# Kernel tuning notes

Measured on AMD Instinct MI355X. Metric: run time of the kernel, lower is better.

Reference implementation:

```python
import jax, jax.numpy as jnp
import numpy as np

B, S, H, NH, I = 8, 1024, 1024, 16, 4096
HD = H // NH
EPS = 1e-6
NEG = -1e9


def _glorot(key, shape):
    lim = np.sqrt(6.0 / (shape[0] + shape[1]))
    return jax.random.uniform(key, shape, jnp.float32, -lim, lim)


def setup_inputs() -> dict:
    key = jax.random.key(0)
    ks = jax.random.split(key, 8)
    return {
        "inputs": jax.random.normal(ks[0], (B, S, H), jnp.float32),
        "inputs_mask": jnp.zeros((B, S), jnp.float32),  # 1.0 marks padding
        "attn_qkvw": _glorot(ks[1], (H, 3 * H)),
        "attn_qkvb": jnp.zeros((3 * H,), jnp.float32),
        "attn_ow": _glorot(ks[2], (H, H)),
        "attn_ob": jnp.zeros((H,), jnp.float32),
        "attn_nw": jnp.ones((H,), jnp.float32),
        "attn_nb": jnp.zeros((H,), jnp.float32),
        "inter_w": _glorot(ks[3], (H, I)),
        "inter_b": jnp.zeros((I,), jnp.float32),
        "output_w": _glorot(ks[4], (I, H)),
        "output_b": jnp.zeros((H,), jnp.float32),
        "ffn_nw": jnp.ones((H,), jnp.float32),
        "ffn_nb": jnp.zeros((H,), jnp.float32),
    }


def _layer_norm(x, g, b):
    m = jnp.mean(x, axis=-1, keepdims=True)
    v = jnp.mean(jnp.square(x - m), axis=-1, keepdims=True)
    return (x - m) * jax.lax.rsqrt(v + EPS) * g + b


def reference(inputs, inputs_mask, attn_qkvw, attn_qkvb, attn_ow, attn_ob,
              attn_nw, attn_nb, inter_w, inter_b, output_w, output_b,
              ffn_nw, ffn_nb):
    # ---- self-attention block (pre-LN) ----
    res = inputs
    x = _layer_norm(inputs, attn_nw, attn_nb)
    qkv = x @ attn_qkvw + attn_qkvb                      # [B,S,3H]
    q, k, v = jnp.split(qkv, 3, axis=-1)
    q = q.reshape(B, S, NH, HD)
    k = k.reshape(B, S, NH, HD)
    v = v.reshape(B, S, NH, HD)
    scale = 1.0 / np.sqrt(HD)
    scores = jnp.einsum("bqhd,bkhd->bhqk", q, k) * scale
    scores = scores + inputs_mask[:, None, None, :] * NEG
    probs = jax.nn.softmax(scores, axis=-1)
    ctx = jnp.einsum("bhqk,bkhd->bqhd", probs, v).reshape(B, S, H)
    attn_out = ctx @ attn_ow + attn_ob
    x = res + attn_out
    # ---- FFN block (pre-LN, ReLU) ----
    res2 = x
    y = _layer_norm(x, ffn_nw, ffn_nb)
    h = jax.nn.relu(y @ inter_w + inter_b)
    return res2 + h @ output_w + output_b
```

## Files before the change

### kernel.cpp

```cpp
#include <hip/hip_runtime.h>
#include <cstdint>
#include <cstddef>

typedef _Float16 f16;
typedef _Float16 half8 __attribute__((ext_vector_type(8)));
typedef _Float16 half4v __attribute__((ext_vector_type(4)));
typedef float floatx4 __attribute__((ext_vector_type(4)));
typedef float floatx16 __attribute__((ext_vector_type(16)));

__device__ __forceinline__ floatx4 mfma16(half8 a, half8 b, floatx4 c) {
    return __builtin_amdgcn_mfma_f32_16x16x32_f16(a, b, c, 0, 0, 0);
}
__device__ __forceinline__ floatx16 mfma32(half8 a, half8 b, floatx16 c) {
    return __builtin_amdgcn_mfma_f32_32x32x16_f16(a, b, c, 0, 0, 0);
}

__device__ __forceinline__ void async16(const f16* g, f16* l) {
    __builtin_amdgcn_global_load_lds(
        (const __attribute__((address_space(1))) unsigned int*)(uintptr_t)g,
        (__attribute__((address_space(3))) unsigned int*)(uintptr_t)l,
        16, 0, 0);
}

__global__ __launch_bounds__(256)
void ln_f16_kernel(const float* __restrict__ x, const float* __restrict__ g,
                   const float* __restrict__ be, f16* __restrict__ y)
{
    int row = blockIdx.x, t = threadIdx.x;
    const float* xr = x + (size_t)row * 1024;
    float4 v = *(const float4*)(xr + t * 4);
    float s1 = v.x + v.y + v.z + v.w;
    float s2 = v.x * v.x + v.y * v.y + v.z * v.z + v.w * v.w;
    #pragma unroll
    for (int off = 32; off >= 1; off >>= 1) {
        s1 += __shfl_xor(s1, off);
        s2 += __shfl_xor(s2, off);
    }
    __shared__ float r1[4], r2[4];
    if ((t & 63) == 0) { r1[t >> 6] = s1; r2[t >> 6] = s2; }
    __syncthreads();
    s1 = r1[0] + r1[1] + r1[2] + r1[3];
    s2 = r2[0] + r2[1] + r2[2] + r2[3];
    float mean = s1 * 0.0009765625f;
    float var  = s2 * 0.0009765625f - mean * mean;
    float rs = rsqrtf(var + 1e-6f);
    float4 gv = *(const float4*)(g + t * 4);
    float4 bv = *(const float4*)(be + t * 4);
    half4v o;
    o[0] = (f16)((v.x - mean) * rs * gv.x + bv.x);
    o[1] = (f16)((v.y - mean) * rs * gv.y + bv.y);
    o[2] = (f16)((v.z - mean) * rs * gv.z + bv.z);
    o[3] = (f16)((v.w - mean) * rs * gv.w + bv.w);
    *(half4v*)(y + (size_t)row * 1024 + t * 4) = o;
}

__global__ __launch_bounds__(256)
void transpose_f16_kernel(const float* __restrict__ W, f16* __restrict__ WT,
                          int R, int C)
{
    __shared__ float tile[32][33];
    int tx = threadIdx.x & 31, ty0 = threadIdx.x >> 5;
    int r0 = blockIdx.y * 32, c0 = blockIdx.x * 32;
    #pragma unroll
    for (int i = 0; i < 4; ++i)
        tile[ty0 + i * 8][tx] = W[(size_t)(r0 + ty0 + i * 8) * C + c0 + tx];
    __syncthreads();
    #pragma unroll
    for (int i = 0; i < 4; ++i)
        WT[(size_t)(c0 + ty0 + i * 8) * R + r0 + tx] = (f16)tile[tx][ty0 + i * 8];
}

__global__ __launch_bounds__(256, 2)
void gemm_kernel(const f16* __restrict__ A, const f16* __restrict__ BT,
                 const float* __restrict__ bias, const float* __restrict__ res,
                 float* __restrict__ Cf32, int M, int N, int K)
{
    __shared__ __align__(16) f16 As[128 * 64];
    __shared__ __align__(16) f16 Bs[128 * 64];
    int m0 = blockIdx.x * 128, n0 = blockIdx.y * 128;
    int t = threadIdx.x, lane = t & 63, wave = t >> 6;
    int quad = lane >> 4, l16 = lane & 15;
    int wm = (wave & 1) * 64, wn = (wave >> 1) * 64;
    int sw = l16 & 7;
    floatx4 acc[4][4] = {};

    for (int k0 = 0; k0 < K; k0 += 64) {
        __syncthreads();
        #pragma unroll
        for (int c = 0; c < 4; ++c) {
            int s = c * 256 + t;
            int row = s >> 3, phys = s & 7;
            int lg = phys ^ (row & 7);
            async16(A  + (size_t)(m0 + row) * K + k0 + lg * 8,
                    As + (size_t)(c * 256 + (t & ~63)) * 8);
            async16(BT + (size_t)(n0 + row) * K + k0 + lg * 8,
                    Bs + (size_t)(c * 256 + (t & ~63)) * 8);
        }
        __syncthreads();
        #pragma unroll
        for (int ks = 0; ks < 2; ++ks) {
            int ca = (ks * 4 + quad) ^ sw;
            half8 a[4], b[4];
            #pragma unroll
            for (int i = 0; i < 4; ++i) {
                a[i] = *(const half8*)(As + (wm + i * 16 + l16) * 64 + ca * 8);
                b[i] = *(const half8*)(Bs + (wn + i * 16 + l16) * 64 + ca * 8);
            }
            #pragma unroll
            for (int i = 0; i < 4; ++i)
                #pragma unroll
                for (int j = 0; j < 4; ++j)
                    acc[i][j] = mfma16(a[i], b[j], acc[i][j]);
        }
    }

    #pragma unroll
    for (int j = 0; j < 4; ++j) {
        int col = n0 + wn + j * 16 + l16;
        float bv = bias[col];
        #pragma unroll
        for (int i = 0; i < 4; ++i) {
            int rowb = m0 + wm + i * 16 + quad * 4;
            #pragma unroll
            for (int r = 0; r < 4; ++r) {
                float v = acc[i][j][r] + bv;
                size_t idx = (size_t)(rowb + r) * N + col;
                Cf32[idx] = v + res[idx];
            }
        }
    }
}

template<int MODE>
__global__ __launch_bounds__(256, 2)
void gemm_big_kernel(const f16* __restrict__ A, const f16* __restrict__ BT,
                     const float* __restrict__ bias, f16* __restrict__ Cf16,
                     f16* __restrict__ qb, f16* __restrict__ kb, f16* __restrict__ vb,
                     int M, int N, int K)
{
    __shared__ __align__(16) f16 As[256 * 64];
    __shared__ __align__(16) f16 Bs[128 * 64];
    int m0 = blockIdx.x * 256, n0 = blockIdx.y * 128;
    int t = threadIdx.x, lane = t & 63, wave = t >> 6;
    int l32 = lane & 31, kg = lane >> 5;
    int swz = l32 & 7;
    floatx16 acc[2][4];
    #pragma unroll
    for (int mi = 0; mi < 2; ++mi)
        #pragma unroll
        for (int jn = 0; jn < 4; ++jn)
            #pragma unroll
            for (int r = 0; r < 16; ++r) acc[mi][jn][r] = 0.f;

    for (int k0 = 0; k0 < K; k0 += 64) {
        __syncthreads();
        #pragma unroll
        for (int c = 0; c < 8; ++c) {
            int s = c * 256 + t;
            int row = s >> 3, phys = s & 7;
            int lg = phys ^ (row & 7);
            async16(A + (size_t)(m0 + row) * K + k0 + lg * 8,
                    As + (size_t)(c * 256 + (t & ~63)) * 8);
        }
        #pragma unroll
        for (int c = 0; c < 4; ++c) {
            int s = c * 256 + t;
            int row = s >> 3, phys = s & 7;
            int lg = phys ^ (row & 7);
            async16(BT + (size_t)(n0 + row) * K + k0 + lg * 8,
                    Bs + (size_t)(c * 256 + (t & ~63)) * 8);
        }
        __syncthreads();
        #pragma unroll
        for (int ss = 0; ss < 4; ++ss) {
            int ca = (ss * 2 + kg) ^ swz;
            half8 a[2], b[4];
            #pragma unroll
            for (int mi = 0; mi < 2; ++mi)
                a[mi] = *(const half8*)(As + (wave * 64 + mi * 32 + l32) * 64 + ca * 8);
            #pragma unroll
            for (int jn = 0; jn < 4; ++jn)
                b[jn] = *(const half8*)(Bs + (jn * 32 + l32) * 64 + ca * 8);
            #pragma unroll
            for (int mi = 0; mi < 2; ++mi)
                #pragma unroll
                for (int jn = 0; jn < 4; ++jn)
                    acc[mi][jn] = mfma32(a[mi], b[jn], acc[mi][jn]);
        }
    }

    #pragma unroll
    for (int mi = 0; mi < 2; ++mi) {
        int mbase = m0 + wave * 64 + mi * 32 + 4 * kg;
        #pragma unroll
        for (int jn = 0; jn < 4; ++jn) {
            int col = n0 + jn * 32 + l32;
            float bv = bias[col];
            if (MODE == 1) {
                #pragma unroll
                for (int reg = 0; reg < 16; ++reg) {
                    int row = mbase + (reg & 3) + 8 * (reg >> 2);
                    Cf16[(size_t)row * N + col] = (f16)fmaxf(acc[mi][jn][reg] + bv, 0.f);
                }
            } else {
                int part = col >> 10;
                int h = (col >> 6) & 15;
                int d = col & 63;
                if (part == 2) {
                    #pragma unroll
                    for (int rb = 0; rb < 4; ++rb) {
                        int m = mbase + 8 * rb;
                        int bb = m >> 10, s = m & 1023;
                        size_t bh = (size_t)bb * 16 + h;
                        half4v pv;
                        #pragma unroll
                        for (int r = 0; r < 4; ++r) pv[r] = (f16)(acc[mi][jn][rb * 4 + r] + bv);
                        *(half4v*)(vb + (bh * 64 + d) * 1024 + s) = pv;
                    }
                } else {
                    f16* dst0 = part == 0 ? qb : kb;
                    #pragma unroll
                    for (int reg = 0; reg < 16; ++reg) {
                        int m = mbase + (reg & 3) + 8 * (reg >> 2);
                        int bb = m >> 10, s = m & 1023;
                        size_t bh = (size_t)bb * 16 + h;
                        dst0[(bh * 1024 + s) * 64 + d] = (f16)(acc[mi][jn][reg] + bv);
                    }
                }
            }
        }
    }
}

__global__ __launch_bounds__(256)
void attn_kernel(const f16* __restrict__ qb, const f16* __restrict__ kb,
                 const f16* __restrict__ vb, const float* __restrict__ mask,
                 f16* __restrict__ ctx)
{
    const int S = 1024;
    int qt = blockIdx.x, h = blockIdx.y, b = blockIdx.z;
    size_t bh = (size_t)b * 16 + h;
    int t = threadIdx.x, lane = t & 63, wv = t >> 6;
    int quad = lane >> 4, l16 = lane & 15;
    int sw = l16 & 7;

    __shared__ __align__(16) f16 Ks[64 * 64];
    __shared__ __align__(16) f16 Vs[64 * 64];
    __shared__ __align__(16) f16 Ps[4][16 * 40];

    int q0 = qt * 64 + wv * 16;
    const f16* qrow = qb + (bh * 1024 + q0 + l16) * 64;
    half8 aq0 = *(const half8*)(qrow + quad * 8);
    half8 aq1 = *(const half8*)(qrow + 32 + quad * 8);

    floatx4 o[4] = {};
    float lsum[4] = {0.f, 0.f, 0.f, 0.f};
    const float scale = 0.125f;
    const float* mrow = mask + b * S;

    for (int kc = 0; kc < S; kc += 64) {
        __syncthreads();
        #pragma unroll
        for (int c = 0; c < 2; ++c) {
            int s = c * 256 + t;
            int row = s >> 3, phys = s & 7;
            int lg = phys ^ (row & 7);
            f16* lk = Ks + (size_t)(c * 256 + (t & ~63)) * 8;
            f16* lv = Vs + (size_t)(c * 256 + (t & ~63)) * 8;
            async16(kb + (bh * 1024 + kc + row) * 64 + lg * 8, lk);
            async16(vb + (bh * 64 + row) * 1024 + kc + lg * 8, lv);
        }
        __syncthreads();

        floatx4 sf[4];
        #pragma unroll
        for (int cg = 0; cg < 4; ++cg) {
            const f16* kr = Ks + (cg * 16 + l16) * 64;
            int c0 = quad ^ sw;
            half8 b0 = *(const half8*)(kr + c0 * 8);
            half8 b1 = *(const half8*)(kr + (c0 ^ 4) * 8);
            floatx4 z = {};
            sf[cg] = mfma16(aq1, b1, mfma16(aq0, b0, z));
        }
        #pragma unroll
        for (int cg = 0; cg < 4; ++cg) {
            float mk = mrow[kc + cg * 16 + l16] * (-1e9f);
            #pragma unroll
            for (int r = 0; r < 4; ++r) {
                float e = __expf(sf[cg][r] * scale + mk);
                lsum[r] += e;
                Ps[wv][(quad * 4 + r) * 40 + cg * 16 + l16] = (f16)e;
            }
        }
        half8 ap0 = *(const half8*)(Ps[wv] + l16 * 40 + quad * 8);
        half8 ap1 = *(const half8*)(Ps[wv] + l16 * 40 + 32 + quad * 8);
        #pragma unroll
        for (int td = 0; td < 4; ++td) {
            const f16* vr = Vs + (td * 16 + l16) * 64;
            int c0 = quad ^ sw;
            half8 bv0 = *(const half8*)(vr + c0 * 8);
            half8 bv1 = *(const half8*)(vr + (c0 ^ 4) * 8);
            o[td] = mfma16(ap0, bv0, o[td]);
            o[td] = mfma16(ap1, bv1, o[td]);
        }
    }

    #pragma unroll
    for (int r = 0; r < 4; ++r) {
        float s = lsum[r];
        s += __shfl_xor(s, 1); s += __shfl_xor(s, 2);
        s += __shfl_xor(s, 4); s += __shfl_xor(s, 8);
        lsum[r] = 1.f / s;
    }
    #pragma unroll
    for (int td = 0; td < 4; ++td)
        #pragma unroll
        for (int r = 0; r < 4; ++r)
            ctx[((size_t)b * 1024 + q0 + quad * 4 + r) * 1024 + h * 64 + td * 16 + l16]
                = (f16)(o[td][r] * lsum[r]);
}

extern "C" void kernel_launch(void* const* d_in, const int* in_sizes, int n_in,
                              void* d_out, int out_size, void* d_ws, size_t ws_size,
                              hipStream_t stream)
{
    const float* inputs = (const float*)d_in[0];
    const float* mask   = (const float*)d_in[1];
    const float* qkvw   = (const float*)d_in[2];
    const float* qkvb   = (const float*)d_in[3];
    const float* ow     = (const float*)d_in[4];
    const float* ob     = (const float*)d_in[5];
    const float* anw    = (const float*)d_in[6];
    const float* anb    = (const float*)d_in[7];
    const float* iw     = (const float*)d_in[8];
    const float* ib     = (const float*)d_in[9];
    const float* outw   = (const float*)d_in[10];
    const float* outb   = (const float*)d_in[11];
    const float* fnw    = (const float*)d_in[12];
    const float* fnb    = (const float*)d_in[13];
    float* out = (float*)d_out;

    const int M = 8192;
    uint8_t* ws = (uint8_t*)d_ws;
    f16* wT_qkv = (f16*)(ws + 0);
    f16* wT_o   = (f16*)(ws + 6291456);
    f16* wT_i   = (f16*)(ws + 8388608);
    f16* wT_out = (f16*)(ws + 16777216);
    f16* xln    = (f16*)(ws + 25165824);
    float* x1   = (float*)(ws + 41943040);
    f16* qbuf   = (f16*)(ws + 75497472);
    f16* kbuf   = (f16*)(ws + 92274688);
    f16* vbuf   = (f16*)(ws + 109051904);
    f16* ctx    = (f16*)(ws + 125829120);
    f16* hbuf   = (f16*)(ws + 75497472);

    transpose_f16_kernel<<<dim3(96, 32),  256, 0, stream>>>(qkvw, wT_qkv, 1024, 3072);
    transpose_f16_kernel<<<dim3(32, 32),  256, 0, stream>>>(ow,   wT_o,   1024, 1024);
    transpose_f16_kernel<<<dim3(128, 32), 256, 0, stream>>>(iw,   wT_i,   1024, 4096);
    transpose_f16_kernel<<<dim3(32, 128), 256, 0, stream>>>(outw, wT_out, 4096, 1024);

    ln_f16_kernel<<<8192, 256, 0, stream>>>(inputs, anw, anb, xln);

    gemm_big_kernel<2><<<dim3(32, 24), 256, 0, stream>>>(xln, wT_qkv, qkvb,
        nullptr, qbuf, kbuf, vbuf, M, 3072, 1024);

    attn_kernel<<<dim3(16, 16, 8), 256, 0, stream>>>(qbuf, kbuf, vbuf, mask, ctx);

    gemm_kernel<<<dim3(64, 8), 256, 0, stream>>>(ctx, wT_o, ob, inputs,
        x1, M, 1024, 1024);

    ln_f16_kernel<<<8192, 256, 0, stream>>>(x1, fnw, fnb, xln);

    gemm_big_kernel<1><<<dim3(32, 32), 256, 0, stream>>>(xln, wT_i, ib,
        hbuf, nullptr, nullptr, nullptr, M, 4096, 1024);

    gemm_kernel<<<dim3(64, 8), 256, 0, stream>>>(hbuf, wT_out, outb, x1,
        out, M, 1024, 4096);
}
```

Before: 482.3 us.

## Replace GEMMs with triple-buffered 512-thread pipelined MFMA kernel

Replaces both GEMM kernels with one templated kernel that uses 8 waves, a 256x128 tile and a three-stage LDS ring. Async global-to-LDS loads for tile k+2 are interleaved with the MFMA phases of tile k, using explicit barriers, setprio and waitcnt. The aim is to hide global load latency that the old load-sync-compute loop exposed, and to unify the epilogues. In exchange it uses more LDS per block (144KB with three stages), which may limit occupancy, and the hand-placed barriers and waitcnts add synchronisation risk. The output-projection GEMMs now launch fewer, larger blocks (256), which may underfill the CUs.

```diff
diff --git a/kernel.cpp b/kernel.cpp
--- a/kernel.cpp
+++ b/kernel.cpp
@@ -70,160 +70,144 @@
         WT[(size_t)(c0 + ty0 + i * 8) * R + r0 + tx] = (f16)tile[tx][ty0 + i * 8];
 }
 
-__global__ __launch_bounds__(256, 2)
-void gemm_kernel(const f16* __restrict__ A, const f16* __restrict__ BT,
-                 const float* __restrict__ bias, const float* __restrict__ res,
-                 float* __restrict__ Cf32, int M, int N, int K)
-{
-    __shared__ __align__(16) f16 As[128 * 64];
-    __shared__ __align__(16) f16 Bs[128 * 64];
-    int m0 = blockIdx.x * 128, n0 = blockIdx.y * 128;
-    int t = threadIdx.x, lane = t & 63, wave = t >> 6;
-    int quad = lane >> 4, l16 = lane & 15;
-    int wm = (wave & 1) * 64, wn = (wave >> 1) * 64;
-    int sw = l16 & 7;
-    floatx4 acc[4][4] = {};
-
-    for (int k0 = 0; k0 < K; k0 += 64) {
-        __syncthreads();
-        #pragma unroll
-        for (int c = 0; c < 4; ++c) {
-            int s = c * 256 + t;
-            int row = s >> 3, phys = s & 7;
-            int lg = phys ^ (row & 7);
-            async16(A  + (size_t)(m0 + row) * K + k0 + lg * 8,
-                    As + (size_t)(c * 256 + (t & ~63)) * 8);
-            async16(BT + (size_t)(n0 + row) * K + k0 + lg * 8,
-                    Bs + (size_t)(c * 256 + (t & ~63)) * 8);
-        }
-        __syncthreads();
-        #pragma unroll
-        for (int ks = 0; ks < 2; ++ks) {
-            int ca = (ks * 4 + quad) ^ sw;
-            half8 a[4], b[4];
+#define GPHASE(aoff, boff, ss, ...) do {                                        \
+    const int ci_ = ((ss) * 2 + kg) ^ swz;                                      \
+    half8 fa0 = *(const half8*)(AS + (aoff) + (wm +      l32) * 64 + ci_ * 8);  \
+    half8 fa1 = *(const half8*)(AS + (aoff) + (wm + 32 + l32) * 64 + ci_ * 8);  \
+    half8 fb0 = *(const half8*)(BS + (boff) + (wn +      l32) * 64 + ci_ * 8);  \
+    half8 fb1 = *(const half8*)(BS + (boff) + (wn + 32 + l32) * 64 + ci_ * 8);  \
+    __VA_ARGS__                                                                 \
+    __builtin_amdgcn_s_barrier();                                               \
+    asm volatile("s_waitcnt lgkmcnt(0)" ::: "memory");                          \
+    __builtin_amdgcn_sched_barrier(0);                                          \
+    __builtin_amdgcn_s_setprio(1);                                              \
+    acc[0][0] = mfma32(fa0, fb0, acc[0][0]);                                    \
+    acc[0][1] = mfma32(fa0, fb1, acc[0][1]);                                    \
+    acc[1][0] = mfma32(fa1, fb0, acc[1][0]);                                    \
+    acc[1][1] = mfma32(fa1, fb1, acc[1][1]);                                    \
+    __builtin_amdgcn_s_setprio(0);                                              \
+    __builtin_amdgcn_s_barrier();                                               \
+} while (0)
+
+template<int MODE>
+__global__ __launch_bounds__(512, 2)
+void gemm_pipe_kernel(const f16* __restrict__ A, const f16* __restrict__ BT,
+                      const float* __restrict__ bias, const float* __restrict__ res,
+                      float* __restrict__ Cf32, f16* __restrict__ Cf16,
+                      f16* __restrict__ qb, f16* __restrict__ kb, f16* __restrict__ vb,
+                      int M, int N, int K)
+{
+    __shared__ __align__(16) f16 AS[3 * 256 * 64];
+    __shared__ __align__(16) f16 BS[3 * 128 * 64];
+    const int m0 = blockIdx.x * 256, n0 = blockIdx.y * 128;
+    const int t = threadIdx.x, lane = t & 63, wave = t >> 6;
+    const int l32 = lane & 31, kg = lane >> 5, swz = l32 & 7;
+    const int wm = (wave >> 1) * 64, wn = (wave & 1) * 64;
+
+    floatx16 acc[2][2];
+    #pragma unroll
+    for (int i = 0; i < 2; ++i)
+        #pragma unroll
+        for (int j = 0; j < 2; ++j)
             #pragma unroll
-            for (int i = 0; i < 4; ++i) {
-                a[i] = *(const half8*)(As + (wm + i * 16 + l16) * 64 + ca * 8);
-                b[i] = *(const half8*)(Bs + (wn + i * 16 + l16) * 64 + ca * 8);
-            }
-            #pragma unroll
-            for (int i = 0; i < 4; ++i)
-                #pragma unroll
-                for (int j = 0; j < 4; ++j)
-                    acc[i][j] = mfma16(a[i], b[j], acc[i][j]);
-        }
-    }
-
-    #pragma unroll
-    for (int j = 0; j < 4; ++j) {
-        int col = n0 + wn + j * 16 + l16;
-        float bv = bias[col];
-        #pragma unroll
-        for (int i = 0; i < 4; ++i) {
-            int rowb = m0 + wm + i * 16 + quad * 4;
-            #pragma unroll
-            for (int r = 0; r < 4; ++r) {
-                float v = acc[i][j][r] + bv;
-                size_t idx = (size_t)(rowb + r) * N + col;
-                Cf32[idx] = v + res[idx];
-            }
-        }
-    }
-}
-
-template<int MODE>
-__global__ __launch_bounds__(256, 2)
-void gemm_big_kernel(const f16* __restrict__ A, const f16* __restrict__ BT,
-                     const float* __restrict__ bias, f16* __restrict__ Cf16,
-                     f16* __restrict__ qb, f16* __restrict__ kb, f16* __restrict__ vb,
-                     int M, int N, int K)
-{
-    __shared__ __align__(16) f16 As[256 * 64];
-    __shared__ __align__(16) f16 Bs[128 * 64];
-    int m0 = blockIdx.x * 256, n0 = blockIdx.y * 128;
-    int t = threadIdx.x, lane = t & 63, wave = t >> 6;
-    int l32 = lane & 31, kg = lane >> 5;
-    int swz = l32 & 7;
-    floatx16 acc[2][4];
-    #pragma unroll
-    for (int mi = 0; mi < 2; ++mi)
-        #pragma unroll
-        for (int jn = 0; jn < 4; ++jn)
-            #pragma unroll
-            for (int r = 0; r < 16; ++r) acc[mi][jn][r] = 0.f;
-
-    for (int k0 = 0; k0 < K; k0 += 64) {
-        __syncthreads();
-        #pragma unroll
-        for (int c = 0; c < 8; ++c) {
-            int s = c * 256 + t;
-            int row = s >> 3, phys = s & 7;
-            int lg = phys ^ (row & 7);
-            async16(A + (size_t)(m0 + row) * K + k0 + lg * 8,
-                    As + (size_t)(c * 256 + (t & ~63)) * 8);
-        }
-        #pragma unroll
-        for (int c = 0; c < 4; ++c) {
-            int s = c * 256 + t;
-            int row = s >> 3, phys = s & 7;
-            int lg = phys ^ (row & 7);
-            async16(BT + (size_t)(n0 + row) * K + k0 + lg * 8,
-                    Bs + (size_t)(c * 256 + (t & ~63)) * 8);
-        }
-        __syncthreads();
-        #pragma unroll
-        for (int ss = 0; ss < 4; ++ss) {
-            int ca = (ss * 2 + kg) ^ swz;
-            half8 a[2], b[4];
-            #pragma unroll
-            for (int mi = 0; mi < 2; ++mi)
-                a[mi] = *(const half8*)(As + (wave * 64 + mi * 32 + l32) * 64 + ca * 8);
-            #pragma unroll
-            for (int jn = 0; jn < 4; ++jn)
-                b[jn] = *(const half8*)(Bs + (jn * 32 + l32) * 64 + ca * 8);
-            #pragma unroll
-            for (int mi = 0; mi < 2; ++mi)
-                #pragma unroll
-                for (int jn = 0; jn < 4; ++jn)
-                    acc[mi][jn] = mfma32(a[mi], b[jn], acc[mi][jn]);
-        }
-    }
+            for (int r = 0; r < 16; ++r) acc[i][j][r] = 0.f;
+
+    const f16* gA[4]; int oA[4];
+    #pragma unroll
+    for (int c = 0; c < 4; ++c) {
+        int s = c * 512 + t, row = s >> 3, lg = (s & 7) ^ (row & 7);
+        gA[c] = A + (size_t)(m0 + row) * K + lg * 8;
+        oA[c] = (c * 512 + (t & ~63)) * 8;
+    }
+    const f16* gB[2]; int oB[2];
+    #pragma unroll
+    for (int c = 0; c < 2; ++c) {
+        int s = c * 512 + t, row = s >> 3, lg = (s & 7) ^ (row & 7);
+        gB[c] = BT + (size_t)(n0 + row) * K + lg * 8;
+        oB[c] = (c * 512 + (t & ~63)) * 8;
+    }
+
+    int ac = 0, an = 16384, as_ = 32768;
+    int bc = 0, bn = 8192,  bs_ = 16384;
+
+    #pragma unroll
+    for (int c = 0; c < 4; ++c) async16(gA[c], AS + ac + oA[c]);
+    #pragma unroll
+    for (int c = 0; c < 2; ++c) async16(gB[c], BS + bc + oB[c]);
+    #pragma unroll
+    for (int c = 0; c < 4; ++c) async16(gA[c] + 64, AS + an + oA[c]);
+    #pragma unroll
+    for (int c = 0; c < 2; ++c) async16(gB[c] + 64, BS + bn + oB[c]);
+    asm volatile("s_waitcnt vmcnt(6)" ::: "memory");
+    __builtin_amdgcn_s_barrier();
+
+    const int NT = K >> 6;
+    #pragma unroll 1
+    for (int it = 0; it < NT - 2; ++it) {
+        const int k2 = (it + 2) << 6;
+        GPHASE(ac, bc, 0, async16(gA[0] + k2, AS + as_ + oA[0]);
+                          async16(gA[1] + k2, AS + as_ + oA[1]); );
+        GPHASE(ac, bc, 1, async16(gA[2] + k2, AS + as_ + oA[2]);
+                          async16(gA[3] + k2, AS + as_ + oA[3]); );
+        GPHASE(ac, bc, 2, async16(gB[0] + k2, BS + bs_ + oB[0]);
+                          async16(gB[1] + k2, BS + bs_ + oB[1]); );
+        GPHASE(ac, bc, 3, );
+        asm volatile("s_waitcnt vmcnt(6)" ::: "memory");
+        __builtin_amdgcn_s_barrier();
+        int tp = ac; ac = an; an = as_; as_ = tp;
+        tp = bc; bc = bn; bn = bs_; bs_ = tp;
+    }
+    GPHASE(ac, bc, 0, ); GPHASE(ac, bc, 1, );
+    GPHASE(ac, bc, 2, ); GPHASE(ac, bc, 3, );
+    asm volatile("s_waitcnt vmcnt(0)" ::: "memory");
+    __builtin_amdgcn_s_barrier();
+    ac = an; bc = bn;
+    GPHASE(ac, bc, 0, ); GPHASE(ac, bc, 1, );
+    GPHASE(ac, bc, 2, ); GPHASE(ac, bc, 3, );
 
     #pragma unroll
     for (int mi = 0; mi < 2; ++mi) {
-        int mbase = m0 + wave * 64 + mi * 32 + 4 * kg;
-        #pragma unroll
-        for (int jn = 0; jn < 4; ++jn) {
-            int col = n0 + jn * 32 + l32;
-            float bv = bias[col];
-            if (MODE == 1) {
+        const int mbase = m0 + wm + mi * 32 + 4 * kg;
+        #pragma unroll
+        for (int jn = 0; jn < 2; ++jn) {
+            const int col = n0 + wn + jn * 32 + l32;
+            const float bv = bias[col];
+            if (MODE == 0) {
                 #pragma unroll
                 for (int reg = 0; reg < 16; ++reg) {
-                    int row = mbase + (reg & 3) + 8 * (reg >> 2);
+                    const int row = mbase + (reg & 3) + 8 * (reg >> 2);
+                    const size_t idx = (size_t)row * N + col;
+                    Cf32[idx] = acc[mi][jn][reg] + bv + res[idx];
+                }
+            } else if (MODE == 1) {
+                #pragma unroll
+                for (int reg = 0; reg < 16; ++reg) {
+                    const int row = mbase + (reg & 3) + 8 * (reg >> 2);
                     Cf16[(size_t)row * N + col] = (f16)fmaxf(acc[mi][jn][reg] + bv, 0.f);
                 }
             } else {
-                int part = col >> 10;
-                int h = (col >> 6) & 15;
-                int d = col & 63;
+                const int part = col >> 10;
+                const int h = (col >> 6) & 15;
+                const int d = col & 63;
                 if (part == 2) {
                     #pragma unroll
                     for (int rb = 0; rb < 4; ++rb) {
-                        int m = mbase + 8 * rb;
-                        int bb = m >> 10, s = m & 1023;
-                        size_t bh = (size_t)bb * 16 + h;
+                        const int m = mbase + 8 * rb;
+                        const int bb = m >> 10, s = m & 1023;
+                        const size_t bh = (size_t)bb * 16 + h;
                         half4v pv;
                         #pragma unroll
-                        for (int r = 0; r < 4; ++r) pv[r] = (f16)(acc[mi][jn][rb * 4 + r] + bv);
+                        for (int r = 0; r < 4; ++r)
+                            pv[r] = (f16)(acc[mi][jn][rb * 4 + r] + bv);
                         *(half4v*)(vb + (bh * 64 + d) * 1024 + s) = pv;
                     }
                 } else {
                     f16* dst0 = part == 0 ? qb : kb;
                     #pragma unroll
                     for (int reg = 0; reg < 16; ++reg) {
-                        int m = mbase + (reg & 3) + 8 * (reg >> 2);
-                        int bb = m >> 10, s = m & 1023;
-                        size_t bh = (size_t)bb * 16 + h;
+                        const int m = mbase + (reg & 3) + 8 * (reg >> 2);
+                        const int bb = m >> 10, s = m & 1023;
+                        const size_t bh = (size_t)bb * 16 + h;
                         dst0[(bh * 1024 + s) * 64 + d] = (f16)(acc[mi][jn][reg] + bv);
                     }
                 }
@@ -361,19 +345,19 @@
 
     ln_f16_kernel<<<8192, 256, 0, stream>>>(inputs, anw, anb, xln);
 
-    gemm_big_kernel<2><<<dim3(32, 24), 256, 0, stream>>>(xln, wT_qkv, qkvb,
-        nullptr, qbuf, kbuf, vbuf, M, 3072, 1024);
+    gemm_pipe_kernel<2><<<dim3(32, 24), 512, 0, stream>>>(xln, wT_qkv, qkvb,
+        nullptr, nullptr, nullptr, qbuf, kbuf, vbuf, M, 3072, 1024);
 
     attn_kernel<<<dim3(16, 16, 8), 256, 0, stream>>>(qbuf, kbuf, vbuf, mask, ctx);
 
-    gemm_kernel<<<dim3(64, 8), 256, 0, stream>>>(ctx, wT_o, ob, inputs,
-        x1, M, 1024, 1024);
+    gemm_pipe_kernel<0><<<dim3(32, 8), 512, 0, stream>>>(ctx, wT_o, ob, inputs,
+        x1, nullptr, nullptr, nullptr, nullptr, M, 1024, 1024);
 
     ln_f16_kernel<<<8192, 256, 0, stream>>>(x1, fnw, fnb, xln);
 
-    gemm_big_kernel<1><<<dim3(32, 32), 256, 0, stream>>>(xln, wT_i, ib,
-        hbuf, nullptr, nullptr, nullptr, M, 4096, 1024);
-
-    gemm_kernel<<<dim3(64, 8), 256, 0, stream>>>(hbuf, wT_out, outb, x1,
-        out, M, 1024, 4096);
-}
+    gemm_pipe_kernel<1><<<dim3(32, 32), 512, 0, stream>>>(xln, wT_i, ib,
+        nullptr, nullptr, hbuf, nullptr, nullptr, nullptr, M, 4096, 1024);
+
+    gemm_pipe_kernel<0><<<dim3(32, 8), 512, 0, stream>>>(hbuf, wT_out, outb, x1,
+        out, nullptr, nullptr, nullptr, nullptr, M, 1024, 4096);
+}
```

New measurement: 489.8 us. Within noise of the previous version (+1.6%).

## Pre-pack B weights into MFMA fragment layout and load them straight into registers

Applied to the files above, without the earlier changes.

Adds a packing kernel that converts the output-projection and FFN-output weights into per-lane MFMA fragment order. A new GEMM kernel then loads B fragments from global memory directly into registers, no longer staging B through LDS. This halves LDS traffic and shared memory per block for those two GEMMs. In exchange, each wave now reads its B fragments from global or L2 memory without reuse across the two M-waves. Those loads are also not overlapped with the LDS staging and could add latency.

```diff
diff --git a/kernel.cpp b/kernel.cpp
--- a/kernel.cpp
+++ b/kernel.cpp
@@ -70,47 +70,82 @@
         WT[(size_t)(c0 + ty0 + i * 8) * R + r0 + tx] = (f16)tile[tx][ty0 + i * 8];
 }
 
+__global__ __launch_bounds__(256)
+void pack_b_kernel(const float* __restrict__ W, f16* __restrict__ Bp, int K, int N)
+{
+    __shared__ float tile[64][65];
+    int n00 = blockIdx.x * 64, k00 = blockIdx.y * 64;
+    int t = threadIdx.x;
+    int tx = t & 63, r0 = t >> 6;
+    #pragma unroll
+    for (int i = 0; i < 16; ++i)
+        tile[r0 + i * 4][tx] = W[(size_t)(k00 + r0 + i * 4) * N + n00 + tx];
+    __syncthreads();
+    const int KC = K >> 5;
+    #pragma unroll
+    for (int it = 0; it < 2; ++it) {
+        int cid = it * 256 + t;
+        int gl = cid >> 7;
+        int cl = (cid >> 6) & 1;
+        int lane = cid & 63;
+        int q = lane >> 4, l16 = lane & 15;
+        int nl = gl * 16 + l16;
+        int kl = cl * 32 + q * 8;
+        half8 v;
+        #pragma unroll
+        for (int i = 0; i < 8; ++i) v[i] = (f16)tile[kl + i][nl];
+        size_t g = (size_t)((n00 >> 4) + gl);
+        size_t c = (size_t)((k00 >> 5) + cl);
+        *(half8*)(Bp + (g * KC + c) * 512 + (size_t)lane * 8) = v;
+    }
+}
+
 __global__ __launch_bounds__(256, 2)
-void gemm_kernel(const f16* __restrict__ A, const f16* __restrict__ BT,
-                 const float* __restrict__ bias, const float* __restrict__ res,
-                 float* __restrict__ Cf32, int M, int N, int K)
+void gemm_breg_kernel(const f16* __restrict__ A, const f16* __restrict__ Bp,
+                      const float* __restrict__ bias, const float* __restrict__ res,
+                      float* __restrict__ Cf32, int M, int N, int K)
 {
     __shared__ __align__(16) f16 As[128 * 64];
-    __shared__ __align__(16) f16 Bs[128 * 64];
     int m0 = blockIdx.x * 128, n0 = blockIdx.y * 128;
     int t = threadIdx.x, lane = t & 63, wave = t >> 6;
     int quad = lane >> 4, l16 = lane & 15;
     int wm = (wave & 1) * 64, wn = (wave >> 1) * 64;
     int sw = l16 & 7;
     floatx4 acc[4][4] = {};
+    const int KC = K >> 5;
+    const int gbase = (n0 + wn) >> 4;
+    const f16* bp0 = Bp + (size_t)lane * 8;
 
     for (int k0 = 0; k0 < K; k0 += 64) {
+        half8 bf[2][4];
+        #pragma unroll
+        for (int ks = 0; ks < 2; ++ks)
+            #pragma unroll
+            for (int j = 0; j < 4; ++j)
+                bf[ks][j] = *(const half8*)(bp0 +
+                    ((size_t)((gbase + j) * KC + (k0 >> 5) + ks) << 9));
         __syncthreads();
         #pragma unroll
         for (int c = 0; c < 4; ++c) {
             int s = c * 256 + t;
             int row = s >> 3, phys = s & 7;
             int lg = phys ^ (row & 7);
-            async16(A  + (size_t)(m0 + row) * K + k0 + lg * 8,
+            async16(A + (size_t)(m0 + row) * K + k0 + lg * 8,
                     As + (size_t)(c * 256 + (t & ~63)) * 8);
-            async16(BT + (size_t)(n0 + row) * K + k0 + lg * 8,
-                    Bs + (size_t)(c * 256 + (t & ~63)) * 8);
         }
         __syncthreads();
         #pragma unroll
         for (int ks = 0; ks < 2; ++ks) {
             int ca = (ks * 4 + quad) ^ sw;
-            half8 a[4], b[4];
-            #pragma unroll
-            for (int i = 0; i < 4; ++i) {
+            half8 a[4];
+            #pragma unroll
+            for (int i = 0; i < 4; ++i)
                 a[i] = *(const half8*)(As + (wm + i * 16 + l16) * 64 + ca * 8);
-                b[i] = *(const half8*)(Bs + (wn + i * 16 + l16) * 64 + ca * 8);
-            }
             #pragma unroll
             for (int i = 0; i < 4; ++i)
                 #pragma unroll
                 for (int j = 0; j < 4; ++j)
-                    acc[i][j] = mfma16(a[i], b[j], acc[i][j]);
+                    acc[i][j] = mfma16(a[i], bf[ks][j], acc[i][j]);
         }
     }
 
@@ -343,9 +378,9 @@
     const int M = 8192;
     uint8_t* ws = (uint8_t*)d_ws;
     f16* wT_qkv = (f16*)(ws + 0);
-    f16* wT_o   = (f16*)(ws + 6291456);
+    f16* Bp_o   = (f16*)(ws + 6291456);
     f16* wT_i   = (f16*)(ws + 8388608);
-    f16* wT_out = (f16*)(ws + 16777216);
+    f16* Bp_out = (f16*)(ws + 16777216);
     f16* xln    = (f16*)(ws + 25165824);
     float* x1   = (float*)(ws + 41943040);
     f16* qbuf   = (f16*)(ws + 75497472);
@@ -355,9 +390,9 @@
     f16* hbuf   = (f16*)(ws + 75497472);
 
     transpose_f16_kernel<<<dim3(96, 32),  256, 0, stream>>>(qkvw, wT_qkv, 1024, 3072);
-    transpose_f16_kernel<<<dim3(32, 32),  256, 0, stream>>>(ow,   wT_o,   1024, 1024);
     transpose_f16_kernel<<<dim3(128, 32), 256, 0, stream>>>(iw,   wT_i,   1024, 4096);
-    transpose_f16_kernel<<<dim3(32, 128), 256, 0, stream>>>(outw, wT_out, 4096, 1024);
+    pack_b_kernel<<<dim3(16, 16), 256, 0, stream>>>(ow,   Bp_o,   1024, 1024);
+    pack_b_kernel<<<dim3(16, 64), 256, 0, stream>>>(outw, Bp_out, 4096, 1024);
 
     ln_f16_kernel<<<8192, 256, 0, stream>>>(inputs, anw, anb, xln);
 
@@ -366,7 +401,7 @@
 
     attn_kernel<<<dim3(16, 16, 8), 256, 0, stream>>>(qbuf, kbuf, vbuf, mask, ctx);
 
-    gemm_kernel<<<dim3(64, 8), 256, 0, stream>>>(ctx, wT_o, ob, inputs,
+    gemm_breg_kernel<<<dim3(64, 8), 256, 0, stream>>>(ctx, Bp_o, ob, inputs,
         x1, M, 1024, 1024);
 
     ln_f16_kernel<<<8192, 256, 0, stream>>>(x1, fnw, fnb, xln);
@@ -374,6 +409,6 @@
     gemm_big_kernel<1><<<dim3(32, 32), 256, 0, stream>>>(xln, wT_i, ib,
         hbuf, nullptr, nullptr, nullptr, M, 4096, 1024);
 
-    gemm_kernel<<<dim3(64, 8), 256, 0, stream>>>(hbuf, wT_out, outb, x1,
+    gemm_breg_kernel<<<dim3(64, 8), 256, 0, stream>>>(hbuf, Bp_out, outb, x1,
         out, M, 1024, 4096);
 }
```

Result: slower. 504.3 us (+4.6%).
